# Kernel tuning notes

Measured on AMD Instinct MI355X. Metric: run time of the kernel, lower is better.

Reference implementation:

```python
import jax, jax.numpy as jnp
import numpy as np

# ---------- filter construction (setup-time, numpy) ----------

def _conv2full(A, B):
    out = np.zeros((A.shape[0] + B.shape[0] - 1, A.shape[1] + B.shape[1] - 1))
    for i in range(B.shape[0]):
        for j in range(B.shape[1]):
            out[i:i + A.shape[0], j:j + A.shape[1]] += B[i, j] * A
    return out

def _mctrans(b, t):
    # McClellan transform of 1-D zero-phase filter b through kernel t
    n = (len(b) - 1) // 2
    c = len(b) // 2
    a = np.concatenate([[b[c]], 2.0 * b[c + 1:]])
    P0 = np.array([[1.0]]); P1 = t
    h = a[1] * t
    h[t.shape[0] // 2, t.shape[1] // 2] += a[0]
    for i in range(2, n + 1):
        P2 = 2.0 * _conv2full(t, P1)
        off = ((P2.shape[0] - P0.shape[0]) // 2, (P2.shape[1] - P0.shape[1]) // 2)
        P2[off[0]:off[0] + P0.shape[0], off[1]:off[1] + P0.shape[1]] -= P0
        hn = a[i] * P2
        o2 = ((P2.shape[0] - h.shape[0]) // 2, (P2.shape[1] - h.shape[1]) // 2)
        hn[o2[0]:o2[0] + h.shape[0], o2[1]:o2[1] + h.shape[1]] += h
        h = hn; P0, P1 = P1, P2
    return h

def _make_filters():
    # pyramidal 'maxflat' 1-D analysis pair (pfilters-style), DC gain sqrt(2)
    k1 = 1.0 - np.sqrt(2.0); k2 = 1.0 / np.sqrt(2.0); k3 = k1; M1 = 1.0 / np.sqrt(2.0)
    hh = np.array([0.25 * k2 * k3, 0.5 * k2, 1.0 + 0.5 * k2 * k3]) * M1
    h = np.concatenate([hh, hh[-2::-1]]) * np.sqrt(2.0)          # 5 taps
    gg = np.array([-0.125 * k1 * k2 * k3, 0.25 * k1 * k2,
                   -0.5 * k1 - 0.5 * k3 - 0.375 * k1 * k2 * k3,
                   1.0 + 0.5 * k1 * k2]) * M1
    g = np.concatenate([gg, gg[-2::-1]]) * np.sqrt(2.0)          # 7 taps
    # diamond maxflat lowpass via McClellan transform of Lagrange halfband
    b = np.array([-1., 0., 9., 16., 9., 0., -1.]) / 32.0
    t = np.array([[0., .25, 0.], [.25, 0., .25], [0., .25, 0.]])
    d0 = _mctrans(b, t)                                           # 7x7 diamond LP
    kh, kw = d0.shape
    mm = (-1.0) ** (np.add.outer(np.arange(kh) - kh // 2, np.arange(kw) - kw // 2))
    d1 = d0 * mm                                                  # complementary diamond
    colmod = (-1.0) ** (np.arange(kw) - kw // 2)                  # diamond -> fan
    f0 = d0 * colmod * np.sqrt(2.0)
    f1 = d1 * colmod * np.sqrt(2.0)
    return h, g, f0, f1

# ---------- jax filtering / resampling primitives ----------

def _sepfilt_per(x, f):
    # separable zero-phase filtering with periodic extension; x [B,C,H,W]
    B, C, H, W = x.shape
    L = f.shape[0]; p = L // 2
    k = f.astype(x.dtype)
    y = jnp.pad(x, ((0, 0), (0, 0), (p, p), (0, 0)), mode='wrap').reshape(B * C, 1, H + 2 * p, W)
    y = jax.lax.conv_general_dilated(y, k.reshape(1, 1, L, 1), (1, 1), 'VALID')
    y = jnp.pad(y, ((0, 0), (0, 0), (0, 0), (p, p)), mode='wrap')
    y = jax.lax.conv_general_dilated(y, k.reshape(1, 1, 1, L), (1, 1), 'VALID')
    return y.reshape(B, C, H, W)

def _filt2_per(x, F):
    B, C, H, W = x.shape
    kh, kw = F.shape; ph, pw = kh // 2, kw // 2
    y = jnp.pad(x, ((0, 0), (0, 0), (ph, ph), (pw, pw)), mode='wrap').reshape(B * C, 1, H + 2 * ph, W + 2 * pw)
    y = jax.lax.conv_general_dilated(y, F.reshape(1, 1, kh, kw).astype(x.dtype), (1, 1), 'VALID')
    return y.reshape(B, C, H, W)

def _qdown_r(x):
    # quincunx downsample: periodic row-shear then keep even rows -> [.., H/2, W]
    H, W = x.shape[-2], x.shape[-1]
    idx = (jnp.arange(W)[None, :] + jnp.arange(H)[:, None]) % W
    z = jnp.take_along_axis(x, jnp.broadcast_to(idx, x.shape), axis=-1)
    return z[..., ::2, :]

def _qdown_c(x):
    # quincunx downsample: periodic column-shear then keep even cols -> [.., H, W/2]
    H, W = x.shape[-2], x.shape[-1]
    idx = (jnp.arange(H)[:, None] + jnp.arange(W)[None, :]) % H
    z = jnp.take_along_axis(x, jnp.broadcast_to(idx, x.shape), axis=-2)
    return z[..., ::2]

# ---------- harness entry points ----------

def setup_inputs() -> dict:
    key = jax.random.key(0)
    x = jax.random.normal(key, (8, 96, 256, 256), dtype=jnp.float32)
    h, g, f0, f1 = _make_filters()
    return {
        'x': x,
        'h': jnp.asarray(h, dtype=jnp.float32),
        'g': jnp.asarray(g, dtype=jnp.float32),
        'f0': jnp.asarray(f0, dtype=jnp.float32),
        'f1': jnp.asarray(f1, dtype=jnp.float32),
    }

def reference(x, h, g, f0, f1):
    # pdfbdec with nlevs=[0,2]: one Laplacian-pyramid level + 2-level DFB on highpass
    xf = _sepfilt_per(x, h)
    xlo = xf[:, :, ::2, ::2]                                  # [B,C,H/2,W/2]
    up = jnp.zeros_like(x).at[:, :, ::2, ::2].set(xlo)
    xhi = x - _sepfilt_per(up, g)                             # LP bandpass [B,C,H,W]
    # DFB level 1: fan filters + quincunx ('1r')
    y0 = _qdown_r(_filt2_per(xhi, f0))                        # [B,C,H/2,W]
    y1 = _qdown_r(_filt2_per(xhi, f1))
    # DFB level 2: transposed fans + quincunx ('2c')
    subs = []
    for y in (y0, y1):
        subs.append(_qdown_c(_filt2_per(y, f0.T)))            # [B,C,H/2,W/2]
        subs.append(_qdown_c(_filt2_per(y, f1.T)))
    xhi_dir = jnp.stack(subs, axis=2)                         # [B,C,4,H/2,W/2]
    return xlo, xhi_dir
```

## Files before the change

kernel.cpp:

```cpp
#include <hip/hip_runtime.h>


#define BC 768

__global__ __launch_bounds__(256) void k1_lowpass(
    const float* __restrict__ x, const float* __restrict__ h,
    float* __restrict__ xlo)
{
    int t = threadIdx.x;
    int tid = blockIdx.x * 256 + t;
    int cb = tid & 63;
    int rb = (tid >> 6) & 63;
    int bc = tid >> 12;
    const float* xb = x + (size_t)bc * 65536;

    int colp[4];
    #pragma unroll
    for (int k = 0; k < 4; ++k) colp[k] = (4 * cb - 2 + 2 * k) & 255;

    float a00 = 0.f, a01 = 0.f, a10 = 0.f, a11 = 0.f;
    #pragma unroll
    for (int pr = 0; pr < 7; ++pr) {
        int row = (4 * rb - 2 + pr) & 255;
        const float* xr = xb + row * 256;
        float X[8];
        #pragma unroll
        for (int k = 0; k < 4; ++k) {
            float2 p = *(const float2*)(xr + colp[k]);
            X[2 * k] = p.x; X[2 * k + 1] = p.y;
        }
        float s0 = h[0]*X[0] + h[1]*X[1] + h[2]*X[2] + h[3]*X[3] + h[4]*X[4];
        float s1 = h[0]*X[2] + h[1]*X[3] + h[2]*X[4] + h[3]*X[5] + h[4]*X[6];
        if (pr <= 4) { a00 += h[pr] * s0;     a01 += h[pr] * s1; }
        if (pr >= 2) { a10 += h[pr - 2] * s0; a11 += h[pr - 2] * s1; }
    }
    size_t ob = (size_t)bc * 16384 + (size_t)(2 * rb) * 128 + 2 * cb;
    *(float2*)(xlo + ob)       = make_float2(a00, a01);
    *(float2*)(xlo + ob + 128) = make_float2(a10, a11);
}

__global__ __launch_bounds__(256) void k2_highpass(
    const float* __restrict__ x, const float* __restrict__ g,
    const float* __restrict__ xlo, float* __restrict__ xs)
{
    int t = threadIdx.x;
    int tid = blockIdx.x * 256 + t;
    int ch = tid & 127;
    int rh = (tid >> 7) & 127;
    int bc = tid >> 14;
    const float* lob = xlo + (size_t)bc * 16384;

    int ri[4] = { (rh - 1) & 127, rh, (rh + 1) & 127, (rh + 2) & 127 };
    int ci[4] = { (ch - 1) & 127, ch, (ch + 1) & 127, (ch + 2) & 127 };

    float ce[4], co[4];
    #pragma unroll
    for (int a = 0; a < 4; ++a) {
        const float* lr = lob + ri[a] * 128;
        float L0 = lr[ci[0]], L1 = lr[ci[1]], L2 = lr[ci[2]], L3 = lr[ci[3]];
        ce[a] = g[1]*L0 + g[3]*L1 + g[5]*L2;
        co[a] = g[0]*L0 + g[2]*L1 + g[4]*L2 + g[6]*L3;
    }
    float aee = g[1]*ce[0] + g[3]*ce[1] + g[5]*ce[2];
    float aeo = g[1]*co[0] + g[3]*co[1] + g[5]*co[2];
    float aoe = g[0]*ce[0] + g[2]*ce[1] + g[4]*ce[2] + g[6]*ce[3];
    float aoo = g[0]*co[0] + g[2]*co[1] + g[4]*co[2] + g[6]*co[3];

    size_t base = (size_t)bc * 65536 + (size_t)(2 * rh) * 256 + 2 * ch;
    float2 xe = *(const float2*)(x + base);
    float2 xo = *(const float2*)(x + base + 256);

    float* xsb = xs + (size_t)bc * 65536;
    int re = 2 * rh, ro = 2 * rh + 1;
    int ce0 = (2 * ch - re + 2) & 255;
    int co0 = (2 * ch - ro + 2) & 255;
    *(float2*)(xsb + re * 256 + ce0) = make_float2(xe.x - aee, xe.y - aeo);
    float* rowo = xsb + ro * 256;
    rowo[co0]             = xo.x - aoe;
    rowo[(co0 + 1) & 255] = xo.y - aoo;
}

__global__ __launch_bounds__(1024) void k34_fused(
    const float* __restrict__ xs, const float* __restrict__ f0,
    const float* __restrict__ f1, float* __restrict__ out_hi)
{
    __shared__ float ylds[128 * 256];
    int t = threadIdx.x;
    int yidx = blockIdx.x & 1;
    int bc   = blockIdx.x >> 1;
    const float* xsb = xs + (size_t)bc * 65536;
    const float* fy = yidx ? f1 : f0;

    {
        int wb = t & 63;
        int rg = t >> 6;
        int r0 = rg * 8;
        int c0 = (4 * wb - 4) & 255;

        float acc[8][4];
        #pragma unroll
        for (int lr = 0; lr < 8; ++lr)
            #pragma unroll
            for (int d = 0; d < 4; ++d) acc[lr][d] = 0.f;

        int base = 2 * r0 - 3;
        #pragma unroll
        for (int ro = 0; ro < 21; ++ro) {
            int row = (base + ro + 256) & 255;
            const float* rp = xsb + row * 256;
            float C[16];
            #pragma unroll
            for (int k = 0; k < 4; ++k) {
                float4 v = *(const float4*)(rp + ((c0 + 4 * k) & 255));
                C[4*k] = v.x; C[4*k+1] = v.y; C[4*k+2] = v.z; C[4*k+3] = v.w;
            }
            #pragma unroll
            for (int lr = 0; lr < 8; ++lr) {
                int i = ro - 2 * lr;
                if (i >= 0 && i <= 6) {
                    #pragma unroll
                    for (int j = 0; j < 7; ++j) {
                        float w0 = fy[i * 7 + j];
                        int mb = j - i + 6;
                        #pragma unroll
                        for (int d = 0; d < 4; ++d)
                            acc[lr][d] += w0 * C[d + mb];
                    }
                }
            }
        }
        #pragma unroll
        for (int lr = 0; lr < 8; ++lr) {
            *(float4*)(&ylds[(r0 + lr) * 256 + 4 * wb]) =
                make_float4(acc[lr][0], acc[lr][1], acc[lr][2], acc[lr][3]);
        }
    }
    __syncthreads();

    {
        int cc = t & 127;
        int lh = t >> 7;
        int rbase = (16 * lh + 2 * cc - 3 + 128) & 127;
        int cb64 = (2 * cc - 4) & 255;

        float s0[16], s1[16];
        #pragma unroll
        for (int m = 0; m < 16; ++m) { s0[m] = 0.f; s1[m] = 0.f; }

        #pragma unroll
        for (int RR = 0; RR < 22; ++RR) {
            const float* tr = &ylds[((rbase + RR) & 127) * 256];
            float T[8];
            #pragma unroll
            for (int k = 0; k < 4; ++k) {
                float2 u = *(const float2*)(tr + ((cb64 + 2 * k) & 255));
                T[2*k] = u.x; T[2*k+1] = u.y;
            }
            #pragma unroll
            for (int m = 0; m < 16; ++m) {
                int i = RR - m;
                if (i >= 0 && i <= 6) {
                    #pragma unroll
                    for (int j = 0; j < 7; ++j) {
                        s0[m] += f0[j * 7 + i] * T[j + 1];
                        s1[m] += f1[j * 7 + i] * T[j + 1];
                    }
                }
            }
        }
        #pragma unroll
        for (int m = 0; m < 16; ++m) {
            int hh = 16 * lh + m;
            size_t o = (size_t)bc * 65536 + (size_t)(2 * yidx) * 16384
                     + (size_t)hh * 128 + cc;
            out_hi[o]         = s0[m];
            out_hi[o + 16384] = s1[m];
        }
    }
}

extern "C" void kernel_launch(void* const* d_in, const int* in_sizes, int n_in,
                              void* d_out, int out_size, void* d_ws, size_t ws_size,
                              hipStream_t stream)
{
    const float* x  = (const float*)d_in[0];
    const float* h  = (const float*)d_in[1];
    const float* g  = (const float*)d_in[2];
    const float* f0 = (const float*)d_in[3];
    const float* f1 = (const float*)d_in[4];

    float* out   = (float*)d_out;
    float* xlo   = out;
    float* hireg = out + 12582912;
    float* xsbuf = (float*)d_ws;

    k1_lowpass<<<12288, 256, 0, stream>>>(x, h, xlo);
    k2_highpass<<<49152, 256, 0, stream>>>(x, g, xlo, xsbuf);
    k34_fused<<<1536, 1024, 0, stream>>>(xsbuf, f0, f1, hireg);
}
```

Baseline: 670.4 us.

## Split fused DFB kernel into column-quarter blocks and widen vector loads

The fused directional filter kernel now runs 256-thread blocks, each covering a quarter of the output columns, with a 128x72 LDS tile instead of a full 128x256 plane. The goal is higher occupancy and more blocks in flight, at the cost of recomputing halo columns in the first stage. The highpass kernel now has each thread produce four columns using float2/float4 loads, and the lowpass kernel uses two float4 loads instead of four float2 loads, to cut memory instruction count.

```diff
diff --git a/kernel.cpp b/kernel.cpp
--- a/kernel.cpp
+++ b/kernel.cpp
@@ -14,23 +14,20 @@
     int bc = tid >> 12;
     const float* xb = x + (size_t)bc * 65536;
 
-    int colp[4];
-    #pragma unroll
-    for (int k = 0; k < 4; ++k) colp[k] = (4 * cb - 2 + 2 * k) & 255;
+    int c0 = (4 * cb - 4) & 255;
+    int c4 = (c0 + 4) & 255;
+    int c8 = (c0 + 8) & 255;
 
     float a00 = 0.f, a01 = 0.f, a10 = 0.f, a11 = 0.f;
     #pragma unroll
     for (int pr = 0; pr < 7; ++pr) {
         int row = (4 * rb - 2 + pr) & 255;
         const float* xr = xb + row * 256;
-        float X[8];
-        #pragma unroll
-        for (int k = 0; k < 4; ++k) {
-            float2 p = *(const float2*)(xr + colp[k]);
-            X[2 * k] = p.x; X[2 * k + 1] = p.y;
-        }
-        float s0 = h[0]*X[0] + h[1]*X[1] + h[2]*X[2] + h[3]*X[3] + h[4]*X[4];
-        float s1 = h[0]*X[2] + h[1]*X[3] + h[2]*X[4] + h[3]*X[5] + h[4]*X[6];
+        float4 v0 = *(const float4*)(xr + c0);
+        float4 v1 = *(const float4*)(xr + c4);
+        float X8 = xr[c8];
+        float s0 = h[0]*v0.z + h[1]*v0.w + h[2]*v1.x + h[3]*v1.y + h[4]*v1.z;
+        float s1 = h[0]*v1.x + h[1]*v1.y + h[2]*v1.z + h[3]*v1.w + h[4]*X8;
         if (pr <= 4) { a00 += h[pr] * s0;     a01 += h[pr] * s1; }
         if (pr >= 2) { a10 += h[pr - 2] * s0; a11 += h[pr - 2] * s1; }
     }
@@ -45,57 +42,75 @@
 {
     int t = threadIdx.x;
     int tid = blockIdx.x * 256 + t;
-    int ch = tid & 127;
-    int rh = (tid >> 7) & 127;
-    int bc = tid >> 14;
+    int cw = tid & 63;
+    int rh = (tid >> 6) & 127;
+    int bc = tid >> 13;
     const float* lob = xlo + (size_t)bc * 16384;
 
     int ri[4] = { (rh - 1) & 127, rh, (rh + 1) & 127, (rh + 2) & 127 };
-    int ci[4] = { (ch - 1) & 127, ch, (ch + 1) & 127, (ch + 2) & 127 };
-
-    float ce[4], co[4];
+    int cb0 = (2 * cw - 2) & 127;
+    int cb2 = (2 * cw) & 127;
+    int cb4 = (2 * cw + 2) & 127;
+
+    float ce0[4], co0[4], ce1[4], co1[4];
     #pragma unroll
     for (int a = 0; a < 4; ++a) {
         const float* lr = lob + ri[a] * 128;
-        float L0 = lr[ci[0]], L1 = lr[ci[1]], L2 = lr[ci[2]], L3 = lr[ci[3]];
-        ce[a] = g[1]*L0 + g[3]*L1 + g[5]*L2;
-        co[a] = g[0]*L0 + g[2]*L1 + g[4]*L2 + g[6]*L3;
-    }
-    float aee = g[1]*ce[0] + g[3]*ce[1] + g[5]*ce[2];
-    float aeo = g[1]*co[0] + g[3]*co[1] + g[5]*co[2];
-    float aoe = g[0]*ce[0] + g[2]*ce[1] + g[4]*ce[2] + g[6]*ce[3];
-    float aoo = g[0]*co[0] + g[2]*co[1] + g[4]*co[2] + g[6]*co[3];
-
-    size_t base = (size_t)bc * 65536 + (size_t)(2 * rh) * 256 + 2 * ch;
-    float2 xe = *(const float2*)(x + base);
-    float2 xo = *(const float2*)(x + base + 256);
+        float2 u0 = *(const float2*)(lr + cb0);
+        float2 u1 = *(const float2*)(lr + cb2);
+        float2 u2 = *(const float2*)(lr + cb4);
+        float X1 = u0.y, X2 = u1.x, X3 = u1.y, X4 = u2.x, X5 = u2.y;
+        ce0[a] = g[1]*X1 + g[3]*X2 + g[5]*X3;
+        co0[a] = g[0]*X1 + g[2]*X2 + g[4]*X3 + g[6]*X4;
+        ce1[a] = g[1]*X2 + g[3]*X3 + g[5]*X4;
+        co1[a] = g[0]*X2 + g[2]*X3 + g[4]*X4 + g[6]*X5;
+    }
+    float ae0 = g[1]*ce0[0] + g[3]*ce0[1] + g[5]*ce0[2];
+    float ae1 = g[1]*co0[0] + g[3]*co0[1] + g[5]*co0[2];
+    float ae2 = g[1]*ce1[0] + g[3]*ce1[1] + g[5]*ce1[2];
+    float ae3 = g[1]*co1[0] + g[3]*co1[1] + g[5]*co1[2];
+    float ao0 = g[0]*ce0[0] + g[2]*ce0[1] + g[4]*ce0[2] + g[6]*ce0[3];
+    float ao1 = g[0]*co0[0] + g[2]*co0[1] + g[4]*co0[2] + g[6]*co0[3];
+    float ao2 = g[0]*ce1[0] + g[2]*ce1[1] + g[4]*ce1[2] + g[6]*ce1[3];
+    float ao3 = g[0]*co1[0] + g[2]*co1[1] + g[4]*co1[2] + g[6]*co1[3];
+
+    size_t base = (size_t)bc * 65536 + (size_t)(2 * rh) * 256 + 4 * cw;
+    float4 xe = *(const float4*)(x + base);
+    float4 xo = *(const float4*)(x + base + 256);
 
     float* xsb = xs + (size_t)bc * 65536;
-    int re = 2 * rh, ro = 2 * rh + 1;
-    int ce0 = (2 * ch - re + 2) & 255;
-    int co0 = (2 * ch - ro + 2) & 255;
-    *(float2*)(xsb + re * 256 + ce0) = make_float2(xe.x - aee, xe.y - aeo);
-    float* rowo = xsb + ro * 256;
-    rowo[co0]             = xo.x - aoe;
-    rowo[(co0 + 1) & 255] = xo.y - aoo;
-}
-
-__global__ __launch_bounds__(1024) void k34_fused(
+    int re = 2 * rh;
+    int se = (4 * cw - re + 2) & 255;
+    float* rowe = xsb + re * 256;
+    *(float2*)(rowe + se)             = make_float2(xe.x - ae0, xe.y - ae1);
+    *(float2*)(rowe + ((se + 2) & 255)) = make_float2(xe.z - ae2, xe.w - ae3);
+    int so = (4 * cw - re + 1 + 256) & 255;
+    float* rowo = xsb + (re + 1) * 256;
+    rowo[so]             = xo.x - ao0;
+    rowo[(so + 1) & 255] = xo.y - ao1;
+    rowo[(so + 2) & 255] = xo.z - ao2;
+    rowo[(so + 3) & 255] = xo.w - ao3;
+}
+
+__global__ __launch_bounds__(256, 4) void k34_fused(
     const float* __restrict__ xs, const float* __restrict__ f0,
     const float* __restrict__ f1, float* __restrict__ out_hi)
 {
-    __shared__ float ylds[128 * 256];
+    __shared__ float ylds[128 * 72];
     int t = threadIdx.x;
-    int yidx = blockIdx.x & 1;
-    int bc   = blockIdx.x >> 1;
+    int q    = blockIdx.x & 3;
+    int yidx = (blockIdx.x >> 2) & 1;
+    int bc   = blockIdx.x >> 3;
+    int C0 = 32 * q;
     const float* xsb = xs + (size_t)bc * 65536;
     const float* fy = yidx ? f1 : f0;
 
-    {
-        int wb = t & 63;
-        int rg = t >> 6;
+    for (int task = t; task < 288; task += 256) {
+        int rg = task / 18;
+        int s  = task - rg * 18;
         int r0 = rg * 8;
-        int c0 = (4 * wb - 4) & 255;
+        int w0 = 2 * C0 - 4 + 4 * s;
+        int c0 = (w0 - 4) & 255;
 
         float acc[8][4];
         #pragma unroll
@@ -120,28 +135,29 @@
                 if (i >= 0 && i <= 6) {
                     #pragma unroll
                     for (int j = 0; j < 7; ++j) {
-                        float w0 = fy[i * 7 + j];
+                        float w = fy[i * 7 + j];
                         int mb = j - i + 6;
                         #pragma unroll
                         for (int d = 0; d < 4; ++d)
-                            acc[lr][d] += w0 * C[d + mb];
+                            acc[lr][d] += w * C[d + mb];
                     }
                 }
             }
         }
         #pragma unroll
         for (int lr = 0; lr < 8; ++lr) {
-            *(float4*)(&ylds[(r0 + lr) * 256 + 4 * wb]) =
+            *(float4*)(&ylds[(r0 + lr) * 72 + 4 * s]) =
                 make_float4(acc[lr][0], acc[lr][1], acc[lr][2], acc[lr][3]);
         }
     }
     __syncthreads();
 
     {
-        int cc = t & 127;
-        int lh = t >> 7;
+        int ccl = t & 31;
+        int lh  = t >> 5;
+        int cc  = C0 + ccl;
         int rbase = (16 * lh + 2 * cc - 3 + 128) & 127;
-        int cb64 = (2 * cc - 4) & 255;
+        int cloc = 2 * ccl;
 
         float s0[16], s1[16];
         #pragma unroll
@@ -149,11 +165,11 @@
 
         #pragma unroll
         for (int RR = 0; RR < 22; ++RR) {
-            const float* tr = &ylds[((rbase + RR) & 127) * 256];
+            const float* tr = &ylds[((rbase + RR) & 127) * 72 + cloc];
             float T[8];
             #pragma unroll
             for (int k = 0; k < 4; ++k) {
-                float2 u = *(const float2*)(tr + ((cb64 + 2 * k) & 255));
+                float2 u = *(const float2*)(tr + 2 * k);
                 T[2*k] = u.x; T[2*k+1] = u.y;
             }
             #pragma unroll
@@ -195,6 +211,6 @@
     float* xsbuf = (float*)d_ws;
 
     k1_lowpass<<<12288, 256, 0, stream>>>(x, h, xlo);
-    k2_highpass<<<49152, 256, 0, stream>>>(x, g, xlo, xsbuf);
-    k34_fused<<<1536, 1024, 0, stream>>>(xsbuf, f0, f1, hireg);
-}
+    k2_highpass<<<24576, 256, 0, stream>>>(x, g, xlo, xsbuf);
+    k34_fused<<<6144, 256, 0, stream>>>(xsbuf, f0, f1, hireg);
+}
```

New measurement: 919.4 us. +37.1%, slower.
